# Kernel tuning notes

Hardware: AMD Instinct MI355X
Metric: run time of the kernel (lower is better)

The kernel has to match this reference:

```python
import jax, jax.numpy as jnp
import numpy as np

H_DIM = 64
NUM_SEQS = 4096
LEN_PATTERN = [16, 24, 32, 40, 48, 56, 64, 40]  # cycles; mean 40, max 64


def _make_seq_start_end():
    lens = np.tile(np.array(LEN_PATTERN, dtype=np.int64), NUM_SEQS // len(LEN_PATTERN))
    ends = np.cumsum(lens)
    starts = np.concatenate([[0], ends[:-1]])
    return np.stack([starts, ends], axis=1)  # [S, 2], total N = 163840


def setup_inputs() -> dict:
    key = jax.random.key(0)
    sse = _make_seq_start_end()
    n_total = int(sse[-1, 1])
    h_states = jax.random.normal(key, (1, n_total, H_DIM), dtype=jnp.float32)
    return {"h_states": h_states, "seq_start_end": jnp.asarray(sse)}


def reference(h_states, seq_start_end):
    # seq_start_end is a constant ragged-segment descriptor; use host values
    sse = np.asarray(jax.device_get(seq_start_end))
    starts = sse[:, 0]
    lens = sse[:, 1] - sse[:, 0]
    L = int(lens.max())              # max pedestrians per scene
    H = h_states.reshape(-1, h_states.shape[-1])  # [N, D]
    N, D = H.shape

    pos = np.arange(L)[None, :]                   # [1, L]
    valid = pos < lens[:, None]                   # [S, L] bool
    idx = starts[:, None] + pos                   # [S, L]
    gather_idx = jnp.asarray(np.where(valid, idx, 0))
    valid_j = jnp.asarray(valid)

    Hp = H[gather_idx]                            # [S, L, D] padded segments
    scores = jnp.einsum('sld,smd->slm', Hp, Hp)   # [S, L, L]
    neg = jnp.asarray(-1e30, dtype=scores.dtype)
    scores = jnp.where(valid_j[:, None, :], scores, neg)  # mask padded keys
    attn = jax.nn.softmax(scores, axis=-1)        # softmax over dim=1 of original (keys)
    ctx = jnp.einsum('slm,smd->sld', attn, Hp)    # [S, L, D]

    # scatter padded rows back to flat [N, D]; invalid rows go to dummy slot N
    flat_idx = jnp.asarray(np.where(valid, idx, N).reshape(-1))
    out = jnp.zeros((N + 1, D), dtype=ctx.dtype).at[flat_idx].set(ctx.reshape(-1, D))
    return out[:N]
```

## Files before the change

### kernel.cpp

```cpp
#include <hip/hip_runtime.h>

#define D 64
#define STR 72
#define WAVES 4

typedef __attribute__((ext_vector_type(8))) short bf16x8;
typedef __attribute__((ext_vector_type(4))) float f32x4;
typedef __attribute__((ext_vector_type(4))) unsigned int u32x4;

static __device__ __forceinline__ unsigned short f2bf(float f) {
  unsigned u = __builtin_bit_cast(unsigned, f);
  u += 0x7fffu + ((u >> 16) & 1u);
  return (unsigned short)(u >> 16);
}

#define LDSWAIT() asm volatile("s_waitcnt lgkmcnt(0)" ::: "memory")

__global__ __launch_bounds__(256, 4)
void seq_attn_kernel(const float* __restrict__ h,
                     const int* __restrict__ sse,
                     float* __restrict__ out) {
  __shared__ unsigned short HsAll[WAVES * 64 * STR];

  const int tid = threadIdx.x;
  const int w = tid >> 6;
  const int lane = tid & 63;
  unsigned short* Hs = HsAll + w * (64 * STR);

  const int s = blockIdx.x + gridDim.x * w;
  const int start = sse[2 * s];
  const int L = sse[2 * s + 1] - start;
  const int nt = (L + 15) >> 4;
  const int g = lane >> 4;
  const int c16 = lane & 15;

  {
    const float* src = h + (size_t)start * D;
    const int c4 = c16 * 4;
    float4 va[8], vb[8];
    #pragma unroll
    for (int it = 0; it < 8; ++it) {
      const int r = it * 4 + g;
      const int rc = (r < L) ? r : 0;
      va[it] = *(const float4*)(src + rc * D + c4);
    }
    const bool hi = (L > 32);
    #pragma unroll
    for (int it = 0; it < 8; ++it) {
      const int r = 32 + it * 4 + g;
      const int rc = (r < L) ? r : 0;
      vb[it] = hi ? *(const float4*)(src + rc * D + c4) : make_float4(0.f, 0.f, 0.f, 0.f);
    }
    #pragma unroll
    for (int it = 0; it < 8; ++it) {
      const int r = it * 4 + g;
      const bool ok = (r < L);
      ushort4 wv;
      wv.x = ok ? f2bf(va[it].x) : (unsigned short)0;
      wv.y = ok ? f2bf(va[it].y) : (unsigned short)0;
      wv.z = ok ? f2bf(va[it].z) : (unsigned short)0;
      wv.w = ok ? f2bf(va[it].w) : (unsigned short)0;
      *(ushort4*)&Hs[r * STR + c4] = wv;
    }
    #pragma unroll
    for (int it = 0; it < 8; ++it) {
      const int r = 32 + it * 4 + g;
      const bool ok = (r < L);
      ushort4 wv;
      wv.x = ok ? f2bf(vb[it].x) : (unsigned short)0;
      wv.y = ok ? f2bf(vb[it].y) : (unsigned short)0;
      wv.z = ok ? f2bf(vb[it].z) : (unsigned short)0;
      wv.w = ok ? f2bf(vb[it].w) : (unsigned short)0;
      *(ushort4*)&Hs[r * STR + c4] = wv;
    }
  }
  LDSWAIT();

  bf16x8 hf[4][2];
  #pragma unroll
  for (int t = 0; t < 4; ++t)
    #pragma unroll
    for (int kb = 0; kb < 2; ++kb)
      hf[t][kb] = *(const bf16x8*)&Hs[(t * 16 + c16) * STR + kb * 32 + g * 8];

  bf16x8 vf[4][2];
  #pragma unroll
  for (int t = 0; t < 4; ++t)
    #pragma unroll
    for (int kb = 0; kb < 2; ++kb) {
      u32x4 wv;
      #pragma unroll
      for (int dd = 0; dd < 4; ++dd) {
        const int k0 = kb * 32 + g * 8 + 2 * dd;
        const unsigned lo = Hs[k0 * STR + t * 16 + c16];
        const unsigned hi2 = Hs[(k0 + 1) * STR + t * 16 + c16];
        wv[dd] = lo | (hi2 << 16);
      }
      vf[t][kb] = __builtin_bit_cast(bf16x8, wv);
    }

  #pragma unroll
  for (int ti = 0; ti < 4; ++ti) {
    if (ti >= nt) continue;

    f32x4 acc[4];
    #pragma unroll
    for (int tj = 0; tj < 4; ++tj) {
      f32x4 z = {0.f, 0.f, 0.f, 0.f};
      acc[tj] = z;
    }
    #pragma unroll
    for (int tj = 0; tj < 4; ++tj)
      #pragma unroll
      for (int kb = 0; kb < 2; ++kb)
        acc[tj] = __builtin_amdgcn_mfma_f32_16x16x32_bf16(
            hf[ti][kb], hf[tj][kb], acc[tj], 0, 0, 0);

    float inv[4];
    #pragma unroll
    for (int r = 0; r < 4; ++r) {
      float mx = -1e30f;
      #pragma unroll
      for (int tj = 0; tj < 4; ++tj) {
        const float sv = (tj * 16 + c16 < L) ? acc[tj][r] : -1e30f;
        acc[tj][r] = sv;
        mx = fmaxf(mx, sv);
      }
      #pragma unroll
      for (int off = 1; off < 16; off <<= 1)
        mx = fmaxf(mx, __shfl_xor(mx, off, 64));
      float sum = 0.f;
      #pragma unroll
      for (int tj = 0; tj < 4; ++tj) {
        const float p = __expf(acc[tj][r] - mx);
        acc[tj][r] = p;
        sum += p;
      }
      #pragma unroll
      for (int off = 1; off < 16; off <<= 1)
        sum += __shfl_xor(sum, off, 64);
      inv[r] = 1.0f / sum;
    }

    #pragma unroll
    for (int tj = 0; tj < 4; ++tj)
      #pragma unroll
      for (int r = 0; r < 4; ++r)
        Hs[(ti * 16 + g * 4 + r) * STR + tj * 16 + c16] = f2bf(acc[tj][r]);

    LDSWAIT();

    bf16x8 pf[2];
    #pragma unroll
    for (int kb = 0; kb < 2; ++kb)
      pf[kb] = *(const bf16x8*)&Hs[(ti * 16 + c16) * STR + kb * 32 + g * 8];

    f32x4 o[4];
    #pragma unroll
    for (int tjd = 0; tjd < 4; ++tjd) {
      f32x4 z = {0.f, 0.f, 0.f, 0.f};
      o[tjd] = z;
    }
    #pragma unroll
    for (int tjd = 0; tjd < 4; ++tjd)
      #pragma unroll
      for (int kb = 0; kb < 2; ++kb)
        o[tjd] = __builtin_amdgcn_mfma_f32_16x16x32_bf16(
            pf[kb], vf[tjd][kb], o[tjd], 0, 0, 0);

    #pragma unroll
    for (int r = 0; r < 4; ++r) {
      const int row = ti * 16 + g * 4 + r;
      if (row < L) {
        float* dst = out + (size_t)(start + row) * D;
        const float sc = inv[r];
        #pragma unroll
        for (int tjd = 0; tjd < 4; ++tjd)
          dst[tjd * 16 + c16] = o[tjd][r] * sc;
      }
    }
  }
}

extern "C" void kernel_launch(void* const* d_in, const int* in_sizes, int n_in,
                              void* d_out, int out_size, void* d_ws, size_t ws_size,
                              hipStream_t stream) {
  const float* h = (const float*)d_in[0];
  const int* sse = (const int*)d_in[1];
  float* out = (float*)d_out;
  const int nseq = in_sizes[1] / 2;
  const int nblk = nseq / WAVES;
  seq_attn_kernel<<<nblk, 64 * WAVES, 0, stream>>>(h, sse, out);
}
```

Baseline: 27.93 us.

## Keep softmax probabilities in registers and feed PV via 16x16x16 MFMA

Computes the full score matrix up front, reading it column-wise so each lane's accumulator layout matches the B-operand layout of a 16x16x16 bf16 MFMA. The normalised probabilities are packed to bf16 in registers and used directly in the PV product. This removes the LDS round trip and barrier wait per row tile. It also loads V fragments only for the valid key tiles. In exchange it holds many more accumulator registers live (16 f32x4 for SS plus the packed probabilities), which risks spills or lower occupancy.

```diff
diff --git a/kernel.cpp b/kernel.cpp
--- a/kernel.cpp
+++ b/kernel.cpp
@@ -5,8 +5,10 @@
 #define WAVES 4
 
 typedef __attribute__((ext_vector_type(8))) short bf16x8;
+typedef __attribute__((ext_vector_type(4))) short bf16x4;
 typedef __attribute__((ext_vector_type(4))) float f32x4;
 typedef __attribute__((ext_vector_type(4))) unsigned int u32x4;
+typedef __attribute__((ext_vector_type(2))) unsigned int u32x2;
 
 static __device__ __forceinline__ unsigned short f2bf(float f) {
   unsigned u = __builtin_bit_cast(unsigned, f);
@@ -15,6 +17,14 @@
 }
 
 #define LDSWAIT() asm volatile("s_waitcnt lgkmcnt(0)" ::: "memory")
+
+static __device__ __forceinline__ f32x4 mfma16(bf16x4 a, bf16x4 b, f32x4 c) {
+#if defined(__HIP_DEVICE_COMPILE__)
+  return __builtin_amdgcn_mfma_f32_16x16x16bf16_1k(a, b, c, 0, 0, 0);
+#else
+  return c;
+#endif
+}
 
 __global__ __launch_bounds__(256, 4)
 void seq_attn_kernel(const float* __restrict__ h,
@@ -83,100 +93,99 @@
     for (int kb = 0; kb < 2; ++kb)
       hf[t][kb] = *(const bf16x8*)&Hs[(t * 16 + c16) * STR + kb * 32 + g * 8];
 
-  bf16x8 vf[4][2];
-  #pragma unroll
-  for (int t = 0; t < 4; ++t)
-    #pragma unroll
-    for (int kb = 0; kb < 2; ++kb) {
-      u32x4 wv;
-      #pragma unroll
-      for (int dd = 0; dd < 4; ++dd) {
-        const int k0 = kb * 32 + g * 8 + 2 * dd;
-        const unsigned lo = Hs[k0 * STR + t * 16 + c16];
-        const unsigned hi2 = Hs[(k0 + 1) * STR + t * 16 + c16];
-        wv[dd] = lo | (hi2 << 16);
-      }
-      vf[t][kb] = __builtin_bit_cast(bf16x8, wv);
-    }
-
+  f32x4 SS[4][4];
+  #pragma unroll
+  for (int a = 0; a < 4; ++a)
+    #pragma unroll
+    for (int b = 0; b < 4; ++b) {
+      f32x4 z = {0.f, 0.f, 0.f, 0.f};
+      SS[a][b] = z;
+    }
+  #pragma unroll
+  for (int a = 0; a < 4; ++a)
+    if (a < nt)
+      #pragma unroll
+      for (int b = 0; b < 4; ++b)
+        if (b < nt)
+          #pragma unroll
+          for (int kb = 0; kb < 2; ++kb)
+            SS[a][b] = __builtin_amdgcn_mfma_f32_16x16x32_bf16(
+                hf[a][kb], hf[b][kb], SS[a][b], 0, 0, 0);
+
+  u32x2 pb[4][4];
   #pragma unroll
   for (int ti = 0; ti < 4; ++ti) {
     if (ti >= nt) continue;
-
-    f32x4 acc[4];
+    float lm = -1e30f;
     #pragma unroll
     for (int tj = 0; tj < 4; ++tj) {
-      f32x4 z = {0.f, 0.f, 0.f, 0.f};
-      acc[tj] = z;
-    }
-    #pragma unroll
-    for (int tj = 0; tj < 4; ++tj)
-      #pragma unroll
-      for (int kb = 0; kb < 2; ++kb)
-        acc[tj] = __builtin_amdgcn_mfma_f32_16x16x32_bf16(
-            hf[ti][kb], hf[tj][kb], acc[tj], 0, 0, 0);
-
-    float inv[4];
-    #pragma unroll
-    for (int r = 0; r < 4; ++r) {
-      float mx = -1e30f;
-      #pragma unroll
-      for (int tj = 0; tj < 4; ++tj) {
-        const float sv = (tj * 16 + c16 < L) ? acc[tj][r] : -1e30f;
-        acc[tj][r] = sv;
-        mx = fmaxf(mx, sv);
+      if (tj >= nt) continue;
+      #pragma unroll
+      for (int e = 0; e < 4; ++e) {
+        const int m = 16 * tj + 4 * g + e;
+        const float v = (m < L) ? SS[tj][ti][e] : -1e30f;
+        SS[tj][ti][e] = v;
+        lm = fmaxf(lm, v);
       }
-      #pragma unroll
-      for (int off = 1; off < 16; off <<= 1)
-        mx = fmaxf(mx, __shfl_xor(mx, off, 64));
-      float sum = 0.f;
-      #pragma unroll
-      for (int tj = 0; tj < 4; ++tj) {
-        const float p = __expf(acc[tj][r] - mx);
-        acc[tj][r] = p;
+    }
+    lm = fmaxf(lm, __shfl_xor(lm, 16, 64));
+    lm = fmaxf(lm, __shfl_xor(lm, 32, 64));
+    float sum = 0.f;
+    #pragma unroll
+    for (int tj = 0; tj < 4; ++tj) {
+      if (tj >= nt) continue;
+      #pragma unroll
+      for (int e = 0; e < 4; ++e) {
+        const float p = __expf(SS[tj][ti][e] - lm);
+        SS[tj][ti][e] = p;
         sum += p;
       }
-      #pragma unroll
-      for (int off = 1; off < 16; off <<= 1)
-        sum += __shfl_xor(sum, off, 64);
-      inv[r] = 1.0f / sum;
-    }
-
-    #pragma unroll
-    for (int tj = 0; tj < 4; ++tj)
-      #pragma unroll
-      for (int r = 0; r < 4; ++r)
-        Hs[(ti * 16 + g * 4 + r) * STR + tj * 16 + c16] = f2bf(acc[tj][r]);
-
-    LDSWAIT();
-
-    bf16x8 pf[2];
-    #pragma unroll
-    for (int kb = 0; kb < 2; ++kb)
-      pf[kb] = *(const bf16x8*)&Hs[(ti * 16 + c16) * STR + kb * 32 + g * 8];
-
-    f32x4 o[4];
-    #pragma unroll
-    for (int tjd = 0; tjd < 4; ++tjd) {
-      f32x4 z = {0.f, 0.f, 0.f, 0.f};
-      o[tjd] = z;
-    }
-    #pragma unroll
-    for (int tjd = 0; tjd < 4; ++tjd)
-      #pragma unroll
-      for (int kb = 0; kb < 2; ++kb)
-        o[tjd] = __builtin_amdgcn_mfma_f32_16x16x32_bf16(
-            pf[kb], vf[tjd][kb], o[tjd], 0, 0, 0);
-
-    #pragma unroll
-    for (int r = 0; r < 4; ++r) {
-      const int row = ti * 16 + g * 4 + r;
-      if (row < L) {
-        float* dst = out + (size_t)(start + row) * D;
-        const float sc = inv[r];
-        #pragma unroll
-        for (int tjd = 0; tjd < 4; ++tjd)
-          dst[tjd * 16 + c16] = o[tjd][r] * sc;
+    }
+    sum += __shfl_xor(sum, 16, 64);
+    sum += __shfl_xor(sum, 32, 64);
+    const float inv = 1.0f / sum;
+    #pragma unroll
+    for (int tj = 0; tj < 4; ++tj) {
+      if (tj >= nt) continue;
+      u32x2 pw;
+      pw[0] = (unsigned)f2bf(SS[tj][ti][0] * inv) | ((unsigned)f2bf(SS[tj][ti][1] * inv) << 16);
+      pw[1] = (unsigned)f2bf(SS[tj][ti][2] * inv) | ((unsigned)f2bf(SS[tj][ti][3] * inv) << 16);
+      pb[ti][tj] = pw;
+    }
+  }
+
+  bf16x4 vfB[4][4];
+  #pragma unroll
+  for (int tj = 0; tj < 4; ++tj) {
+    if (tj >= nt) continue;
+    #pragma unroll
+    for (int dt = 0; dt < 4; ++dt) {
+      u32x2 wv;
+      const unsigned e0 = Hs[(16 * tj + 4 * g + 0) * STR + 16 * dt + c16];
+      const unsigned e1 = Hs[(16 * tj + 4 * g + 1) * STR + 16 * dt + c16];
+      const unsigned e2 = Hs[(16 * tj + 4 * g + 2) * STR + 16 * dt + c16];
+      const unsigned e3 = Hs[(16 * tj + 4 * g + 3) * STR + 16 * dt + c16];
+      wv[0] = e0 | (e1 << 16);
+      wv[1] = e2 | (e3 << 16);
+      vfB[tj][dt] = __builtin_bit_cast(bf16x4, wv);
+    }
+  }
+
+  #pragma unroll
+  for (int ti = 0; ti < 4; ++ti) {
+    if (ti >= nt) continue;
+    #pragma unroll
+    for (int dt = 0; dt < 4; ++dt) {
+      f32x4 o = {0.f, 0.f, 0.f, 0.f};
+      #pragma unroll
+      for (int tj = 0; tj < 4; ++tj)
+        if (tj < nt)
+          o = mfma16(__builtin_bit_cast(bf16x4, pb[ti][tj]), vfB[tj][dt], o);
+      #pragma unroll
+      for (int r = 0; r < 4; ++r) {
+        const int row = ti * 16 + g * 4 + r;
+        if (row < L)
+          out[(size_t)(start + row) * D + dt * 16 + c16] = o[r];
       }
     }
   }
```

Result: no change. 27.52 us (-1.5%).
